# Kernel optimization log

Hardware: AMD Instinct MI355X
Metric: run time of the kernel (lower is better)

## Reference

```python
import jax, jax.numpy as jnp
import numpy as np

N = 50000      # nodes
E = 800000     # edges
IN = 128       # input feature dim
H = 4          # attention heads
D = 32         # per-head hidden dim
L = 3          # GAT layers
C = 32         # num classes
SLOPE = 0.2    # leaky relu negative slope


def _glorot(key, shape):
    fan_in, fan_out = shape[0], shape[-1]
    std = np.sqrt(2.0 / (fan_in + fan_out))
    return jax.random.normal(key, shape, dtype=jnp.float32) * std


def setup_inputs() -> dict:
    key = jax.random.key(0)
    ks = jax.random.split(key, 16)
    inp = {
        "x": jax.random.normal(ks[0], (N, IN), dtype=jnp.float32),
        "src": jax.random.randint(ks[1], (E,), 0, N, dtype=jnp.int32),
        "dst": jax.random.randint(ks[2], (E,), 0, N, dtype=jnp.int32),
        # layer 0: in_dim -> H*D
        "W0": _glorot(ks[3], (IN, H * D)),
        "al0": _glorot(ks[4], (H, D)),
        "ar0": _glorot(ks[5], (H, D)),
        # layers 1,2: H*D -> H*D
        "W1": _glorot(ks[6], (H * D, H * D)),
        "al1": _glorot(ks[7], (H, D)),
        "ar1": _glorot(ks[8], (H, D)),
        "W2": _glorot(ks[9], (H * D, H * D)),
        "al2": _glorot(ks[10], (H, D)),
        "ar2": _glorot(ks[11], (H, D)),
        # JK concat projection: L*H*D -> C (bias=False)
        "Wproj": _glorot(ks[12], (L * H * D, C)),
    }
    return inp


def gat_layer(h, W, al, ar, src, dst):
    """DGL-style GATConv (no residual, no dropout), ELU activation."""
    feat = (h @ W).reshape(N, H, D)                      # [N,H,D]
    el = jnp.sum(feat * al, axis=-1)                     # [N,H]
    er = jnp.sum(feat * ar, axis=-1)                     # [N,H]
    e = jax.nn.leaky_relu(el[src] + er[dst], negative_slope=SLOPE)  # [E,H]
    # edge softmax over incoming edges per destination node
    m = jax.lax.stop_gradient(jax.ops.segment_max(e, dst, num_segments=N))
    ex = jnp.exp(e - m[dst])                             # [E,H]
    s = jax.ops.segment_sum(ex, dst, num_segments=N)     # [N,H]
    a = ex / s[dst]                                      # [E,H]
    out = jax.ops.segment_sum(feat[src] * a[:, :, None], dst, num_segments=N)
    return jax.nn.elu(out).reshape(N, H * D)             # flatten(1)


def reference(x, src, dst, W0, al0, ar0, W1, al1, ar1, W2, al2, ar2, Wproj):
    h0 = gat_layer(x, W0, al0, ar0, src, dst)
    h1 = gat_layer(h0, W1, al1, ar1, src, dst)
    h2 = gat_layer(h1, W2, al2, ar2, src, dst)
    emb = jnp.concatenate([h0, h1, h2], axis=1)          # [N, L*H*D]
    logits = emb @ Wproj                                 # [N, C]
    return logits
```

## Files before the change

### kernel.cpp

```cpp
#include <hip/hip_runtime.h>
#include <hip/hip_fp16.h>
#include <math.h>

#define NNODES 50000
#define NEDGES 800000
#define HD     128
#define NHEADS 4
#define DH     32

#define TILE_R 64
#define AKPF   136

#define PTILE  128

#define NBUCK  196
#define BCAP   6144
#define P1_T   512
#define P1_EPB 4096
#define P2_T   512

struct alignas(16) Half8 { __half2 a, b, c, d; };
typedef _Float16 f16x8 __attribute__((ext_vector_type(8)));
typedef float    f32x4 __attribute__((ext_vector_type(4)));
typedef float    f32x8 __attribute__((ext_vector_type(8)));

static __device__ __forceinline__ float lrelu(float x){ return x > 0.f ? x : 0.2f*x; }
static __device__ __forceinline__ float elu(float x){ return x > 0.f ? x : __expf(x) - 1.f; }


__global__ void init_btail_kernel(int* btail){
  int b = blockIdx.x*blockDim.x + threadIdx.x;
  if (b < NBUCK) btail[b] = b*BCAP;
}

__global__ __launch_bounds__(P1_T) void p1_bucket_kernel(
    const int* __restrict__ src, const int* __restrict__ dst,
    int* __restrict__ btail, unsigned int* __restrict__ bstage, int e)
{
  __shared__ int cnt[NBUCK];
  __shared__ int gstart[NBUCK];
  int t = threadIdx.x;
  int base = blockIdx.x * P1_EPB;
  for (int i = t; i < NBUCK; i += P1_T) cnt[i] = 0;
  __syncthreads();
  int s_[8], b_[8], dl_[8];
  #pragma unroll
  for (int j = 0; j < 8; j++){
    int i = base + j*P1_T + t;
    if (i < e){
      int d = dst[i];
      s_[j]  = src[i];
      b_[j]  = d >> 8;
      dl_[j] = d & 255;
      atomicAdd(&cnt[b_[j]], 1);
    } else b_[j] = -1;
  }
  __syncthreads();
  for (int i = t; i < NBUCK; i += P1_T){
    gstart[i] = cnt[i] ? atomicAdd(&btail[i], cnt[i]) : 0;
    cnt[i] = 0;
  }
  __syncthreads();
  #pragma unroll
  for (int j = 0; j < 8; j++){
    if (b_[j] >= 0){
      int p = atomicAdd(&cnt[b_[j]], 1);
      bstage[(size_t)gstart[b_[j]] + p] = ((unsigned)dl_[j] << 16) | (unsigned)s_[j];
    }
  }
}

__global__ void bucket_scan_kernel(const int* __restrict__ btail, int* __restrict__ ebase,
                                   int* __restrict__ rowptr){
  if (blockIdx.x == 0 && threadIdx.x == 0){
    int run = 0;
    for (int b = 0; b < NBUCK; b++){
      ebase[b] = run;
      run += btail[b] - b*BCAP;
    }
    rowptr[NNODES] = run;
  }
}

__global__ __launch_bounds__(P2_T) void p2_csr_kernel(
    const unsigned int* __restrict__ bstage, const int* __restrict__ btail,
    const int* __restrict__ ebase, int* __restrict__ rowptr, int* __restrict__ srcs)
{
  __shared__ unsigned int ebuf[BCAP];
  __shared__ unsigned short sorted[BCAP];
  __shared__ int cnt[256], ofs[256], run[256];
  int b = blockIdx.x, t = threadIdx.x;
  int nE = btail[b] - b*BCAP;
  int gb = ebase[b];
  const unsigned int* bp = bstage + (size_t)b*BCAP;

  for (int i = t; i < 256; i += P2_T) cnt[i] = 0;
  __syncthreads();
  for (int i = t; i < nE; i += P2_T){
    unsigned int v = bp[i];
    ebuf[i] = v;
    atomicAdd(&cnt[v >> 16], 1);
  }
  __syncthreads();
  if (t < 256) ofs[t] = cnt[t];
  __syncthreads();
  for (int off = 1; off < 256; off <<= 1){
    int v = 0;
    if (t < 256 && t >= off) v = ofs[t - off];
    __syncthreads();
    if (t < 256) ofs[t] += v;
    __syncthreads();
  }
  if (t < 256){
    int ex = ofs[t] - cnt[t];
    run[t] = ex;
    int node = b*256 + t;
    if (node < NNODES) rowptr[node] = gb + ex;
  }
  __syncthreads();
  for (int i = t; i < nE; i += P2_T){
    unsigned int v = ebuf[i];
    int p = atomicAdd(&run[v >> 16], 1);
    sorted[p] = (unsigned short)(v & 0xFFFFu);
  }
  __syncthreads();
  for (int i = t; i < nE; i += P2_T)
    srcs[gb + i] = (int)sorted[i];
}

__global__ void wprep_kernel(const float* __restrict__ W0, const float* __restrict__ W1,
                             const float* __restrict__ W2, _Float16* __restrict__ wt){
  int id = blockIdx.x*blockDim.x + threadIdx.x;
  if (id >= 3*16384) return;
  int l = id >> 14, rem = id & 16383;
  int n = rem >> 7, k = rem & 127;
  const float* W = (l==0) ? W0 : (l==1) ? W1 : W2;
  wt[(size_t)l*16384 + n*128 + k] = (_Float16)W[k*128 + n];
}

template<bool FP16IN>
__global__ __launch_bounds__(256) void gemm_feat_kernel(
    const void* __restrict__ hin, int hstride,
    const _Float16* __restrict__ Wt,
    const float* __restrict__ al, const float* __restrict__ ar,
    __half* __restrict__ feat, float* __restrict__ elv, float* __restrict__ erv)
{
  __shared__ __align__(16) _Float16 Ah[TILE_R*AKPF];
  __shared__ __align__(16) _Float16 Wh[HD*AKPF];
  int t = threadIdx.x;
  int w = t >> 6, lane = t & 63;
  int c = lane & 15, quad = lane >> 4;
  int rbase = blockIdx.x * TILE_R;

  f32x4 acc[8];
  #pragma unroll
  for (int ct = 0; ct < 8; ct++) acc[ct] = (f32x4){0.f, 0.f, 0.f, 0.f};

  int arow = t >> 2;
  int akq  = t & 3;
  int an   = rbase + arow;
  if (FP16IN){
    const _Float16* ap = (const _Float16*)hin + (size_t)an*hstride + akq*8;
    #pragma unroll
    for (int kb = 0; kb < HD; kb += 32){
      f16x8 av = (f16x8)((_Float16)0);
      if (an < NNODES) av = *(const f16x8*)(ap + kb);
      *(f16x8*)&Ah[arow*AKPF + kb + akq*8] = av;
    }
  } else {
    const float* ap = (const float*)hin + (size_t)an*hstride + akq*8;
    #pragma unroll
    for (int kb = 0; kb < HD; kb += 32){
      float4 v0 = make_float4(0.f,0.f,0.f,0.f), v1 = v0;
      if (an < NNODES){
        v0 = *(const float4*)(ap + kb);
        v1 = *(const float4*)(ap + kb + 4);
      }
      f16x8 av;
      av[0]=(_Float16)v0.x; av[1]=(_Float16)v0.y; av[2]=(_Float16)v0.z; av[3]=(_Float16)v0.w;
      av[4]=(_Float16)v1.x; av[5]=(_Float16)v1.y; av[6]=(_Float16)v1.z; av[7]=(_Float16)v1.w;
      *(f16x8*)&Ah[arow*AKPF + kb + akq*8] = av;
    }
  }
  int wn = t >> 1;
  int wk = (t & 1) * 16;
  const _Float16* wp = Wt + wn*HD + wk;
  #pragma unroll
  for (int kb = 0; kb < HD; kb += 32){
    *(uint4*)&Wh[wn*AKPF + kb + wk]     = *(const uint4*)(wp + kb);
    *(uint4*)&Wh[wn*AKPF + kb + wk + 8] = *(const uint4*)(wp + kb + 8);
  }
  __syncthreads();

  #pragma unroll
  for (int kb = 0; kb < HD; kb += 32){
    f16x8 afrag = *(const f16x8*)&Ah[(w*16 + c)*AKPF + kb + quad*8];
    #pragma unroll
    for (int ct = 0; ct < 8; ct++){
      f16x8 bfrag = *(const f16x8*)&Wh[(ct*16 + c)*AKPF + kb + quad*8];
      acc[ct] = __builtin_amdgcn_mfma_f32_16x16x32_f16(afrag, bfrag, acc[ct], 0, 0, 0);
    }
  }

  float alv[8], arv[8];
  #pragma unroll
  for (int ct = 0; ct < 8; ct++){
    int idx = (ct >> 1)*DH + (ct & 1)*16 + c;
    alv[ct] = al[idx];
    arv[ct] = ar[idx];
  }
  #pragma unroll
  for (int r = 0; r < 4; r++){
    int n = rbase + w*16 + quad*4 + r;
    float pl[4], pr[4];
    #pragma unroll
    for (int hh = 0; hh < 4; hh++){
      pl[hh] = acc[2*hh][r]*alv[2*hh] + acc[2*hh+1][r]*alv[2*hh+1];
      pr[hh] = acc[2*hh][r]*arv[2*hh] + acc[2*hh+1][r]*arv[2*hh+1];
    }
    #pragma unroll
    for (int hh = 0; hh < 4; hh++){
      pl[hh] += __shfl_xor(pl[hh], 1); pl[hh] += __shfl_xor(pl[hh], 2);
      pl[hh] += __shfl_xor(pl[hh], 4); pl[hh] += __shfl_xor(pl[hh], 8);
      pr[hh] += __shfl_xor(pr[hh], 1); pr[hh] += __shfl_xor(pr[hh], 2);
      pr[hh] += __shfl_xor(pr[hh], 4); pr[hh] += __shfl_xor(pr[hh], 8);
    }
    if (n < NNODES){
      if (c < 4){ elv[n*NHEADS + c] = pl[c]; erv[n*NHEADS + c] = pr[c]; }
      #pragma unroll
      for (int ct = 0; ct < 8; ct++)
        feat[(size_t)n*HD + ct*16 + c] = __float2half_rn(acc[ct][r]);
    }
  }
}

#define MIX2(alo, ahi, pk, aa) \
  asm("v_fma_mix_f32 %0, %2, %3, %0 op_sel:[0,0,0] op_sel_hi:[1,0,0]\n\t" \
      "v_fma_mix_f32 %1, %2, %3, %1 op_sel:[1,0,0] op_sel_hi:[1,0,0]" \
      : "+v"(alo), "+v"(ahi) : "v"(pk), "v"(aa))

__global__ __launch_bounds__(256) void smax_agg_kernel(
    const int* __restrict__ rowptr, const int* __restrict__ srcs,
    const float* __restrict__ elv, const float* __restrict__ erv,
    const __half* __restrict__ feat, __half* __restrict__ emb_out, int n)
{
  int gid = (int)((blockIdx.x*(size_t)blockDim.x + threadIdx.x) >> 3);
  if (gid >= n) return;
  int fl8  = threadIdx.x & 7;
  int fo   = fl8 * 16;
  int head = fl8 >> 1;

  int s0 = rowptr[gid], s1 = rowptr[gid+1];
  float erh = erv[gid*4 + head];

  float acc[16];
  #pragma unroll
  for (int j = 0; j < 16; j++) acc[j] = 0.f;
  float ssum = 0.f;

  const uint4 zq = make_uint4(0,0,0,0);

  int   sA[4], sB[4];
  uint4 qA0[4], qA1[4], qB0[4], qB1[4];
  float eA[4], eB[4];

#define LOADB(base, S, Q0, Q1, EL)                                   \
  {                                                                  \
    _Pragma("unroll")                                                \
    for (int j = 0; j < 4; j++){                                     \
      int ee = (base) + j;                                           \
      S[j] = (ee < s1) ? srcs[ee] : -1;                              \
    }                                                                \
    _Pragma("unroll")                                                \
    for (int j = 0; j < 4; j++){                                     \
      if (S[j] >= 0){                                                \
        const __half* fr = feat + ((size_t)S[j] << 7) + fo;          \
        Q0[j] = *(const uint4*)(fr);                                 \
        Q1[j] = *(const uint4*)(fr + 8);                             \
        EL[j] = elv[S[j]*4 + head];                                  \
      } else { Q0[j] = zq; Q1[j] = zq; EL[j] = 0.f; }                \
    }                                                                \
  }

#define ACCB(S, Q0, Q1, EL)                                          \
  {                                                                  \
    _Pragma("unroll")                                                \
    for (int j = 0; j < 4; j++){                                     \
      float x = EL[j] + erh;                                         \
      float a = (S[j] >= 0) ? __expf(fmaxf(x, 0.2f*x)) : 0.f;        \
      ssum += a;                                                     \
      MIX2(acc[0],  acc[1],  Q0[j].x, a);                            \
      MIX2(acc[2],  acc[3],  Q0[j].y, a);                            \
      MIX2(acc[4],  acc[5],  Q0[j].z, a);                            \
      MIX2(acc[6],  acc[7],  Q0[j].w, a);                            \
      MIX2(acc[8],  acc[9],  Q1[j].x, a);                            \
      MIX2(acc[10], acc[11], Q1[j].y, a);                            \
      MIX2(acc[12], acc[13], Q1[j].z, a);                            \
      MIX2(acc[14], acc[15], Q1[j].w, a);                            \
    }                                                                \
  }

  LOADB(s0, sA, qA0, qA1, eA);
  for (int e = s0; e < s1; e += 8){
    LOADB(e + 4, sB, qB0, qB1, eB);
    ACCB(sA, qA0, qA1, eA);
    LOADB(e + 8, sA, qA0, qA1, eA);
    ACCB(sB, qB0, qB1, eB);
  }
#undef LOADB
#undef ACCB

  float inv = (ssum > 0.f) ? 1.f / ssum : 0.f;
  __half2 hv[8];
  #pragma unroll
  for (int j = 0; j < 8; j++)
    hv[j] = __floats2half2_rn(elu(acc[2*j]*inv), elu(acc[2*j+1]*inv));
  __half* op = emb_out + (size_t)gid*384 + fo;
  *(uint4*)(op)     = *(uint4*)&hv[0];
  *(uint4*)(op + 8) = *(uint4*)&hv[4];
}

__global__ __launch_bounds__(256) void proj_kernel(
    const __half* __restrict__ emb, const float* __restrict__ Wp, float* __restrict__ part)
{
  __shared__ float As[PTILE*36];
  __shared__ float Wl[32*32];
  int t = threadIdx.x;
  int tx = t & 3, ty = t >> 2;
  int rbase = blockIdx.x * PTILE;
  int kstart = blockIdx.y * 192;
  float* pout = part + (size_t)blockIdx.y * NNODES * 32;

  float acc[2][8];
  #pragma unroll
  for (int r = 0; r < 2; r++)
    #pragma unroll
    for (int j = 0; j < 8; j++) acc[r][j] = 0.f;

  for (int kb = kstart; kb < kstart + 192; kb += 32){
    #pragma unroll
    for (int i = 0; i < 2; i++){
      int idx = i*256 + t;
      int row = idx >> 2;
      int kq  = (idx & 3) * 8;
      int gr  = rbase + row;
      f16x8 v = (f16x8)((_Float16)0);
      if (gr < NNODES) v = *(const f16x8*)((const _Float16*)emb + (size_t)gr*384 + kb + kq);
      float4 f0, f1;
      f0.x=(float)v[0]; f0.y=(float)v[1]; f0.z=(float)v[2]; f0.w=(float)v[3];
      f1.x=(float)v[4]; f1.y=(float)v[5]; f1.z=(float)v[6]; f1.w=(float)v[7];
      *(float4*)&As[row*36 + kq]     = f0;
      *(float4*)&As[row*36 + kq + 4] = f1;
    }
    *(float4*)&Wl[t*4] = *(const float4*)(Wp + (size_t)kb*32 + t*4);
    __syncthreads();

    #pragma unroll 8
    for (int k = 0; k < 32; k++){
      float4 b0 = *(const float4*)&Wl[k*32 + tx*8];
      float4 b1 = *(const float4*)&Wl[k*32 + tx*8 + 4];
      #pragma unroll
      for (int r = 0; r < 2; r++){
        float a = As[(ty + 64*r)*36 + k];
        acc[r][0] += a*b0.x; acc[r][1] += a*b0.y;
        acc[r][2] += a*b0.z; acc[r][3] += a*b0.w;
        acc[r][4] += a*b1.x; acc[r][5] += a*b1.y;
        acc[r][6] += a*b1.z; acc[r][7] += a*b1.w;
      }
    }
    __syncthreads();
  }

  #pragma unroll
  for (int r = 0; r < 2; r++){
    int n = rbase + ty + 64*r;
    if (n < NNODES){
      *(float4*)(pout + (size_t)n*32 + tx*8)     = make_float4(acc[r][0], acc[r][1], acc[r][2], acc[r][3]);
      *(float4*)(pout + (size_t)n*32 + tx*8 + 4) = make_float4(acc[r][4], acc[r][5], acc[r][6], acc[r][7]);
    }
  }
}

__global__ void proj_reduce_kernel(const float4* __restrict__ part, float4* __restrict__ out, int n4){
  int i = blockIdx.x*blockDim.x + threadIdx.x;
  if (i >= n4) return;
  float4 a = part[i];
  float4 b = part[n4 + i];
  out[i] = make_float4(a.x + b.x, a.y + b.y, a.z + b.z, a.w + b.w);
}

extern "C" void kernel_launch(void* const* d_in, const int* in_sizes, int n_in,
                              void* d_out, int out_size, void* d_ws, size_t ws_size,
                              hipStream_t stream) {
  const float* x    = (const float*)d_in[0];
  const int*   src  = (const int*)d_in[1];
  const int*   dst  = (const int*)d_in[2];
  const float* Ws_[3]  = { (const float*)d_in[3], (const float*)d_in[6], (const float*)d_in[9]  };
  const float* als[3] = { (const float*)d_in[4], (const float*)d_in[7], (const float*)d_in[10] };
  const float* ars[3] = { (const float*)d_in[5], (const float*)d_in[8], (const float*)d_in[11] };
  const float* Wproj  = (const float*)d_in[12];
  float* out = (float*)d_out;

  char* wptr = (char*)d_ws;
  auto alloc = [&](size_t bytes) -> void* {
    void* p = (void*)wptr; wptr += (bytes + 255) & ~(size_t)255; return p;
  };
  int*      btail      = (int*)     alloc((size_t)NBUCK*4);
  int*      ebase      = (int*)     alloc((size_t)NBUCK*4);
  unsigned* bstage     = (unsigned*)alloc((size_t)NBUCK*BCAP*4);
  int*      rowptr     = (int*)     alloc((size_t)(NNODES+1)*4);
  int*      src_sorted = (int*)     alloc((size_t)NEDGES*4);
  __half*   feat       = (__half*)  alloc((size_t)NNODES*HD*2);
  float*    elv        = (float*)   alloc((size_t)NNODES*NHEADS*4);
  float*    erv        = (float*)   alloc((size_t)NNODES*NHEADS*4);
  __half*   emb        = (__half*)  alloc((size_t)NNODES*384*2);
  float*    part       = (float*)   alloc((size_t)2*NNODES*32*4);
  _Float16* wt         = (_Float16*)alloc((size_t)3*HD*HD*2);

  init_btail_kernel<<<1, 256, 0, stream>>>(btail);
  p1_bucket_kernel<<<(NEDGES + P1_EPB - 1)/P1_EPB, P1_T, 0, stream>>>(
      src, dst, btail, bstage, NEDGES);
  bucket_scan_kernel<<<1, 64, 0, stream>>>(btail, ebase, rowptr);
  p2_csr_kernel<<<NBUCK, P2_T, 0, stream>>>(bstage, btail, ebase, rowptr, src_sorted);

  wprep_kernel<<<(3*HD*HD + 255)/256, 256, 0, stream>>>(Ws_[0], Ws_[1], Ws_[2], wt);

  const int NGB = (NNODES + TILE_R - 1)/TILE_R;
  const int NSMB = (NNODES*8 + 255)/256;
  gemm_feat_kernel<false><<<NGB, 256, 0, stream>>>(
      (const void*)x, 128, wt, als[0], ars[0], feat, elv, erv);
  smax_agg_kernel<<<NSMB, 256, 0, stream>>>(rowptr, src_sorted, elv, erv,
                                            feat, emb, NNODES);
  for (int l = 1; l < 3; l++){
    gemm_feat_kernel<true><<<NGB, 256, 0, stream>>>(
        (const void*)(emb + (size_t)(l-1)*128), 384,
        wt + (size_t)l*HD*HD, als[l], ars[l], feat, elv, erv);
    smax_agg_kernel<<<NSMB, 256, 0, stream>>>(rowptr, src_sorted, elv, erv,
                                              feat, emb + (size_t)l*128, NNODES);
  }

  dim3 pgrid((NNODES + PTILE - 1)/PTILE, 2);
  proj_kernel<<<pgrid, 256, 0, stream>>>(emb, Wproj, part);
  const int OUT4 = NNODES*32/4;
  proj_reduce_kernel<<<(OUT4+255)/256, 256, 0, stream>>>((const float4*)part, (float4*)out, OUT4);
}
```

Measured before the change: 299.5 us.

## Sort nodes by in-degree for load-balanced softmax aggregation

Builds a degree histogram while constructing the CSR, then computes a prefix over degree bins and scatters node ids into a degree-sorted permutation. The aggregation kernel processes nodes in that order, so neighbouring 8-lane groups in a wavefront have similar edge counts and less divergence. The serial bucket scan is also replaced with a parallel shared-memory scan. The cost is two extra small kernels plus an indirection that breaks contiguity of rowptr, erv and output writes.

```diff
diff --git a/kernel.cpp b/kernel.cpp
--- a/kernel.cpp
+++ b/kernel.cpp
@@ -19,6 +19,8 @@
 #define P1_EPB 4096
 #define P2_T   512
 
+#define NDBIN  64
+
 struct alignas(16) Half8 { __half2 a, b, c, d; };
 typedef _Float16 f16x8 __attribute__((ext_vector_type(8)));
 typedef float    f32x4 __attribute__((ext_vector_type(4)));
@@ -28,9 +30,10 @@
 static __device__ __forceinline__ float elu(float x){ return x > 0.f ? x : __expf(x) - 1.f; }
 
 
-__global__ void init_btail_kernel(int* btail){
+__global__ void init_btail_kernel(int* btail, int* gdhist){
   int b = blockIdx.x*blockDim.x + threadIdx.x;
   if (b < NBUCK) btail[b] = b*BCAP;
+  if (b < NDBIN) gdhist[b] = 0;
 }
 
 __global__ __launch_bounds__(P1_T) void p1_bucket_kernel(
@@ -70,31 +73,41 @@
   }
 }
 
-__global__ void bucket_scan_kernel(const int* __restrict__ btail, int* __restrict__ ebase,
-                                   int* __restrict__ rowptr){
-  if (blockIdx.x == 0 && threadIdx.x == 0){
-    int run = 0;
-    for (int b = 0; b < NBUCK; b++){
-      ebase[b] = run;
-      run += btail[b] - b*BCAP;
-    }
-    rowptr[NNODES] = run;
-  }
+__global__ __launch_bounds__(256) void bucket_scan_kernel(
+    const int* __restrict__ btail, int* __restrict__ ebase, int* __restrict__ rowptr)
+{
+  __shared__ int c[256];
+  int t = threadIdx.x;
+  int mine = (t < NBUCK) ? (btail[t] - t*BCAP) : 0;
+  c[t] = mine;
+  __syncthreads();
+  for (int off = 1; off < 256; off <<= 1){
+    int v = 0;
+    if (t >= off) v = c[t - off];
+    __syncthreads();
+    c[t] += v;
+    __syncthreads();
+  }
+  if (t < NBUCK) ebase[t] = c[t] - mine;
+  if (t == NBUCK - 1) rowptr[NNODES] = c[t];
 }
 
 __global__ __launch_bounds__(P2_T) void p2_csr_kernel(
     const unsigned int* __restrict__ bstage, const int* __restrict__ btail,
-    const int* __restrict__ ebase, int* __restrict__ rowptr, int* __restrict__ srcs)
+    const int* __restrict__ ebase, int* __restrict__ rowptr, int* __restrict__ srcs,
+    int* __restrict__ gdhist)
 {
   __shared__ unsigned int ebuf[BCAP];
   __shared__ unsigned short sorted[BCAP];
   __shared__ int cnt[256], ofs[256], run[256];
+  __shared__ int dh[NDBIN];
   int b = blockIdx.x, t = threadIdx.x;
   int nE = btail[b] - b*BCAP;
   int gb = ebase[b];
   const unsigned int* bp = bstage + (size_t)b*BCAP;
 
   for (int i = t; i < 256; i += P2_T) cnt[i] = 0;
+  if (t < NDBIN) dh[t] = 0;
   __syncthreads();
   for (int i = t; i < nE; i += P2_T){
     unsigned int v = bp[i];
@@ -115,9 +128,14 @@
     int ex = ofs[t] - cnt[t];
     run[t] = ex;
     int node = b*256 + t;
-    if (node < NNODES) rowptr[node] = gb + ex;
-  }
-  __syncthreads();
+    if (node < NNODES){
+      rowptr[node] = gb + ex;
+      int dbin = cnt[t] > NDBIN-1 ? NDBIN-1 : cnt[t];
+      atomicAdd(&dh[dbin], 1);
+    }
+  }
+  __syncthreads();
+  if (t < NDBIN && dh[t]) atomicAdd(&gdhist[t], dh[t]);
   for (int i = t; i < nE; i += P2_T){
     unsigned int v = ebuf[i];
     int p = atomicAdd(&run[v >> 16], 1);
@@ -126,6 +144,44 @@
   __syncthreads();
   for (int i = t; i < nE; i += P2_T)
     srcs[gb + i] = (int)sorted[i];
+}
+
+__global__ void dprefix_kernel(const int* __restrict__ gdhist, int* __restrict__ run){
+  __shared__ int c[NDBIN];
+  int t = threadIdx.x;
+  int mine = gdhist[t];
+  c[t] = mine;
+  __syncthreads();
+  for (int off = 1; off < NDBIN; off <<= 1){
+    int v = 0;
+    if (t >= off) v = c[t - off];
+    __syncthreads();
+    c[t] += v;
+    __syncthreads();
+  }
+  run[t] = c[t] - mine;
+}
+
+__global__ __launch_bounds__(256) void perm_scatter_kernel(
+    const int* __restrict__ rowptr, int* __restrict__ run, int* __restrict__ perm)
+{
+  __shared__ int lh[NDBIN], bb[NDBIN];
+  int t = threadIdx.x, node = blockIdx.x*256 + t;
+  if (t < NDBIN) lh[t] = 0;
+  __syncthreads();
+  int dbin = -1;
+  if (node < NNODES){
+    int d = rowptr[node+1] - rowptr[node];
+    dbin = d > NDBIN-1 ? NDBIN-1 : d;
+    atomicAdd(&lh[dbin], 1);
+  }
+  __syncthreads();
+  if (t < NDBIN){ bb[t] = lh[t] ? atomicAdd(&run[t], lh[t]) : 0; lh[t] = 0; }
+  __syncthreads();
+  if (dbin >= 0){
+    int r = atomicAdd(&lh[dbin], 1);
+    perm[bb[dbin] + r] = node;
+  }
 }
 
 __global__ void wprep_kernel(const float* __restrict__ W0, const float* __restrict__ W1,
@@ -241,11 +297,13 @@
 
 __global__ __launch_bounds__(256) void smax_agg_kernel(
     const int* __restrict__ rowptr, const int* __restrict__ srcs,
+    const int* __restrict__ perm,
     const float* __restrict__ elv, const float* __restrict__ erv,
     const __half* __restrict__ feat, __half* __restrict__ emb_out, int n)
 {
-  int gid = (int)((blockIdx.x*(size_t)blockDim.x + threadIdx.x) >> 3);
-  if (gid >= n) return;
+  int g = (int)((blockIdx.x*(size_t)blockDim.x + threadIdx.x) >> 3);
+  if (g >= n) return;
+  int gid = perm[g];
   int fl8  = threadIdx.x & 7;
   int fo   = fl8 * 16;
   int head = fl8 >> 1;
@@ -416,12 +474,17 @@
   __half*   emb        = (__half*)  alloc((size_t)NNODES*384*2);
   float*    part       = (float*)   alloc((size_t)2*NNODES*32*4);
   _Float16* wt         = (_Float16*)alloc((size_t)3*HD*HD*2);
-
-  init_btail_kernel<<<1, 256, 0, stream>>>(btail);
+  int*      gdhist     = (int*)     alloc((size_t)NDBIN*4);
+  int*      drun       = (int*)     alloc((size_t)NDBIN*4);
+  int*      perm       = (int*)     alloc((size_t)NNODES*4);
+
+  init_btail_kernel<<<1, 256, 0, stream>>>(btail, gdhist);
   p1_bucket_kernel<<<(NEDGES + P1_EPB - 1)/P1_EPB, P1_T, 0, stream>>>(
       src, dst, btail, bstage, NEDGES);
-  bucket_scan_kernel<<<1, 64, 0, stream>>>(btail, ebase, rowptr);
-  p2_csr_kernel<<<NBUCK, P2_T, 0, stream>>>(bstage, btail, ebase, rowptr, src_sorted);
+  bucket_scan_kernel<<<1, 256, 0, stream>>>(btail, ebase, rowptr);
+  p2_csr_kernel<<<NBUCK, P2_T, 0, stream>>>(bstage, btail, ebase, rowptr, src_sorted, gdhist);
+  dprefix_kernel<<<1, NDBIN, 0, stream>>>(gdhist, drun);
+  perm_scatter_kernel<<<NBUCK, 256, 0, stream>>>(rowptr, drun, perm);
 
   wprep_kernel<<<(3*HD*HD + 255)/256, 256, 0, stream>>>(Ws_[0], Ws_[1], Ws_[2], wt);
 
@@ -429,13 +492,13 @@
   const int NSMB = (NNODES*8 + 255)/256;
   gemm_feat_kernel<false><<<NGB, 256, 0, stream>>>(
       (const void*)x, 128, wt, als[0], ars[0], feat, elv, erv);
-  smax_agg_kernel<<<NSMB, 256, 0, stream>>>(rowptr, src_sorted, elv, erv,
+  smax_agg_kernel<<<NSMB, 256, 0, stream>>>(rowptr, src_sorted, perm, elv, erv,
                                             feat, emb, NNODES);
   for (int l = 1; l < 3; l++){
     gemm_feat_kernel<true><<<NGB, 256, 0, stream>>>(
         (const void*)(emb + (size_t)(l-1)*128), 384,
         wt + (size_t)l*HD*HD, als[l], ars[l], feat, elv, erv);
-    smax_agg_kernel<<<NSMB, 256, 0, stream>>>(rowptr, src_sorted, elv, erv,
+    smax_agg_kernel<<<NSMB, 256, 0, stream>>>(rowptr, src_sorted, perm, elv, erv,
                                               feat, emb + (size_t)l*128, NNODES);
   }
 
```

After: 304.8 us. Within noise of the previous version (+1.8%).

## Use MFMA for final projection, fuse weight prep and parallelize bucket scan

Applied to the files above, without the earlier changes.

Replaces the scalar FP32 split-K projection plus its reduce kernel with a single MFMA fp16 kernel that keeps the whole transposed projection weight in shared memory and writes output directly. Merges btail init, layer weight transposition and projection weight conversion into one prep kernel. Replaces the single-thread bucket scan with a 256-thread shared-memory scan. These cut launches, the partial-sum buffer traffic and scalar FMA cost, at the price of fp16 weight rounding for the projection.

```diff
diff --git a/kernel.cpp b/kernel.cpp
--- a/kernel.cpp
+++ b/kernel.cpp
@@ -11,8 +11,6 @@
 #define TILE_R 64
 #define AKPF   136
 
-#define PTILE  128
-
 #define NBUCK  196
 #define BCAP   6144
 #define P1_T   512
@@ -27,11 +25,24 @@
 static __device__ __forceinline__ float lrelu(float x){ return x > 0.f ? x : 0.2f*x; }
 static __device__ __forceinline__ float elu(float x){ return x > 0.f ? x : __expf(x) - 1.f; }
 
-
-__global__ void init_btail_kernel(int* btail){
-  int b = blockIdx.x*blockDim.x + threadIdx.x;
-  if (b < NBUCK) btail[b] = b*BCAP;
-}
+__global__ void prep_kernel(const float* __restrict__ W0, const float* __restrict__ W1,
+                            const float* __restrict__ W2, const float* __restrict__ Wp,
+                            _Float16* __restrict__ wt, _Float16* __restrict__ wt2,
+                            int* __restrict__ btail){
+  int id = blockIdx.x*blockDim.x + threadIdx.x;
+  if (id < NBUCK) btail[id] = id*BCAP;
+  if (id < 3*16384){
+    int l = id >> 14, rem = id & 16383;
+    int n = rem >> 7, k = rem & 127;
+    const float* W = (l==0) ? W0 : (l==1) ? W1 : W2;
+    wt[(size_t)l*16384 + n*128 + k] = (_Float16)W[k*128 + n];
+  } else if (id < 3*16384 + 12288){
+    int rem = id - 3*16384;
+    int k = rem >> 5, n = rem & 31;
+    wt2[n*384 + k] = (_Float16)Wp[k*32 + n];
+  }
+}
+
 
 __global__ __launch_bounds__(P1_T) void p1_bucket_kernel(
     const int* __restrict__ src, const int* __restrict__ dst,
@@ -70,16 +81,23 @@
   }
 }
 
-__global__ void bucket_scan_kernel(const int* __restrict__ btail, int* __restrict__ ebase,
-                                   int* __restrict__ rowptr){
-  if (blockIdx.x == 0 && threadIdx.x == 0){
-    int run = 0;
-    for (int b = 0; b < NBUCK; b++){
-      ebase[b] = run;
-      run += btail[b] - b*BCAP;
-    }
-    rowptr[NNODES] = run;
-  }
+__global__ __launch_bounds__(256) void bucket_scan_kernel(
+    const int* __restrict__ btail, int* __restrict__ ebase, int* __restrict__ rowptr)
+{
+  __shared__ int c[256];
+  int t = threadIdx.x;
+  int mine = (t < NBUCK) ? (btail[t] - t*BCAP) : 0;
+  c[t] = mine;
+  __syncthreads();
+  for (int off = 1; off < 256; off <<= 1){
+    int v = 0;
+    if (t >= off) v = c[t - off];
+    __syncthreads();
+    c[t] += v;
+    __syncthreads();
+  }
+  if (t < NBUCK) ebase[t] = c[t] - mine;
+  if (t == NBUCK - 1) rowptr[NNODES] = c[t];
 }
 
 __global__ __launch_bounds__(P2_T) void p2_csr_kernel(
@@ -126,16 +144,6 @@
   __syncthreads();
   for (int i = t; i < nE; i += P2_T)
     srcs[gb + i] = (int)sorted[i];
-}
-
-__global__ void wprep_kernel(const float* __restrict__ W0, const float* __restrict__ W1,
-                             const float* __restrict__ W2, _Float16* __restrict__ wt){
-  int id = blockIdx.x*blockDim.x + threadIdx.x;
-  if (id >= 3*16384) return;
-  int l = id >> 14, rem = id & 16383;
-  int n = rem >> 7, k = rem & 127;
-  const float* W = (l==0) ? W0 : (l==1) ? W1 : W2;
-  wt[(size_t)l*16384 + n*128 + k] = (_Float16)W[k*128 + n];
 }
 
 template<bool FP16IN>
@@ -320,73 +328,68 @@
   *(uint4*)(op + 8) = *(uint4*)&hv[4];
 }
 
-__global__ __launch_bounds__(256) void proj_kernel(
-    const __half* __restrict__ emb, const float* __restrict__ Wp, float* __restrict__ part)
-{
-  __shared__ float As[PTILE*36];
-  __shared__ float Wl[32*32];
+__global__ __launch_bounds__(256) void proj_mfma_kernel(
+    const __half* __restrict__ emb, const _Float16* __restrict__ Wt2,
+    float* __restrict__ out)
+{
+  __shared__ __align__(16) _Float16 Ah[128*136];
+  __shared__ __align__(16) _Float16 Bh[32*392];
   int t = threadIdx.x;
-  int tx = t & 3, ty = t >> 2;
-  int rbase = blockIdx.x * PTILE;
-  int kstart = blockIdx.y * 192;
-  float* pout = part + (size_t)blockIdx.y * NNODES * 32;
-
-  float acc[2][8];
-  #pragma unroll
-  for (int r = 0; r < 2; r++)
-    #pragma unroll
-    for (int j = 0; j < 8; j++) acc[r][j] = 0.f;
-
-  for (int kb = kstart; kb < kstart + 192; kb += 32){
-    #pragma unroll
-    for (int i = 0; i < 2; i++){
+  int w = t >> 6, lane = t & 63;
+  int c = lane & 15, quad = lane >> 4;
+  int rbase = blockIdx.x * 128;
+
+  f32x4 acc[2][2];
+  #pragma unroll
+  for (int rt = 0; rt < 2; rt++)
+    #pragma unroll
+    for (int ct = 0; ct < 2; ct++) acc[rt][ct] = (f32x4){0.f,0.f,0.f,0.f};
+
+  #pragma unroll
+  for (int i = 0; i < 6; i++){
+    int idx = i*256 + t;
+    int row = idx / 48;
+    int q8  = idx - row*48;
+    *(f16x8*)&Bh[row*392 + q8*8] = *(const f16x8*)(Wt2 + row*384 + q8*8);
+  }
+
+  for (int kc = 0; kc < 384; kc += 128){
+    #pragma unroll
+    for (int i = 0; i < 8; i++){
       int idx = i*256 + t;
-      int row = idx >> 2;
-      int kq  = (idx & 3) * 8;
+      int row = idx >> 4;
+      int q   = idx & 15;
       int gr  = rbase + row;
       f16x8 v = (f16x8)((_Float16)0);
-      if (gr < NNODES) v = *(const f16x8*)((const _Float16*)emb + (size_t)gr*384 + kb + kq);
-      float4 f0, f1;
-      f0.x=(float)v[0]; f0.y=(float)v[1]; f0.z=(float)v[2]; f0.w=(float)v[3];
-      f1.x=(float)v[4]; f1.y=(float)v[5]; f1.z=(float)v[6]; f1.w=(float)v[7];
-      *(float4*)&As[row*36 + kq]     = f0;
-      *(float4*)&As[row*36 + kq + 4] = f1;
-    }
-    *(float4*)&Wl[t*4] = *(const float4*)(Wp + (size_t)kb*32 + t*4);
-    __syncthreads();
-
-    #pragma unroll 8
-    for (int k = 0; k < 32; k++){
-      float4 b0 = *(const float4*)&Wl[k*32 + tx*8];
-      float4 b1 = *(const float4*)&Wl[k*32 + tx*8 + 4];
+      if (gr < NNODES) v = *(const f16x8*)((const _Float16*)emb + (size_t)gr*384 + kc + q*8);
+      *(f16x8*)&Ah[row*136 + q*8] = v;
+    }
+    __syncthreads();
+    #pragma unroll
+    for (int kb = 0; kb < 128; kb += 32){
       #pragma unroll
-      for (int r = 0; r < 2; r++){
-        float a = As[(ty + 64*r)*36 + k];
-        acc[r][0] += a*b0.x; acc[r][1] += a*b0.y;
-        acc[r][2] += a*b0.z; acc[r][3] += a*b0.w;
-        acc[r][4] += a*b1.x; acc[r][5] += a*b1.y;
-        acc[r][6] += a*b1.z; acc[r][7] += a*b1.w;
+      for (int rt = 0; rt < 2; rt++){
+        f16x8 afrag = *(const f16x8*)&Ah[(w*32 + rt*16 + c)*136 + kb + quad*8];
+        #pragma unroll
+        for (int ct = 0; ct < 2; ct++){
+          f16x8 bfrag = *(const f16x8*)&Bh[(ct*16 + c)*392 + kc + kb + quad*8];
+          acc[rt][ct] = __builtin_amdgcn_mfma_f32_16x16x32_f16(afrag, bfrag, acc[rt][ct], 0, 0, 0);
+        }
       }
     }
     __syncthreads();
   }
 
   #pragma unroll
-  for (int r = 0; r < 2; r++){
-    int n = rbase + ty + 64*r;
-    if (n < NNODES){
-      *(float4*)(pout + (size_t)n*32 + tx*8)     = make_float4(acc[r][0], acc[r][1], acc[r][2], acc[r][3]);
-      *(float4*)(pout + (size_t)n*32 + tx*8 + 4) = make_float4(acc[r][4], acc[r][5], acc[r][6], acc[r][7]);
-    }
-  }
-}
-
-__global__ void proj_reduce_kernel(const float4* __restrict__ part, float4* __restrict__ out, int n4){
-  int i = blockIdx.x*blockDim.x + threadIdx.x;
-  if (i >= n4) return;
-  float4 a = part[i];
-  float4 b = part[n4 + i];
-  out[i] = make_float4(a.x + b.x, a.y + b.y, a.z + b.z, a.w + b.w);
+  for (int rt = 0; rt < 2; rt++)
+    #pragma unroll
+    for (int r = 0; r < 4; r++){
+      int n = rbase + w*32 + rt*16 + quad*4 + r;
+      if (n < NNODES){
+        out[(size_t)n*32 + c]      = acc[rt][0][r];
+        out[(size_t)n*32 + 16 + c] = acc[rt][1][r];
+      }
+    }
 }
 
 extern "C" void kernel_launch(void* const* d_in, const int* in_sizes, int n_in,
@@ -414,16 +417,16 @@
   float*    elv        = (float*)   alloc((size_t)NNODES*NHEADS*4);
   float*    erv        = (float*)   alloc((size_t)NNODES*NHEADS*4);
   __half*   emb        = (__half*)  alloc((size_t)NNODES*384*2);
-  float*    part       = (float*)   alloc((size_t)2*NNODES*32*4);
   _Float16* wt         = (_Float16*)alloc((size_t)3*HD*HD*2);
-
-  init_btail_kernel<<<1, 256, 0, stream>>>(btail);
+  _Float16* wt2        = (_Float16*)alloc((size_t)32*384*2);
+
+  prep_kernel<<<(3*16384 + 12288 + 255)/256, 256, 0, stream>>>(
+      Ws_[0], Ws_[1], Ws_[2], Wproj, wt, wt2, btail);
+
   p1_bucket_kernel<<<(NEDGES + P1_EPB - 1)/P1_EPB, P1_T, 0, stream>>>(
       src, dst, btail, bstage, NEDGES);
-  bucket_scan_kernel<<<1, 64, 0, stream>>>(btail, ebase, rowptr);
+  bucket_scan_kernel<<<1, 256, 0, stream>>>(btail, ebase, rowptr);
   p2_csr_kernel<<<NBUCK, P2_T, 0, stream>>>(bstage, btail, ebase, rowptr, src_sorted);
-
-  wprep_kernel<<<(3*HD*HD + 255)/256, 256, 0, stream>>>(Ws_[0], Ws_[1], Ws_[2], wt);
 
   const int NGB = (NNODES + TILE_R - 1)/TILE_R;
   const int NSMB = (NNODES*8 + 255)/256;
@@ -439,8 +442,5 @@
                                               feat, emb + (size_t)l*128, NNODES);
   }
 
-  dim3 pgrid((NNODES + PTILE - 1)/PTILE, 2);
-  proj_kernel<<<pgrid, 256, 0, stream>>>(emb, Wproj, part);
-  const int OUT4 = NNODES*32/4;
-  proj_reduce_kernel<<<(OUT4+255)/256, 256, 0, stream>>>((const float4*)part, (float4*)out, OUT4);
-}
+  proj_mfma_kernel<<<(NNODES + 127)/128, 256, 0, stream>>>(emb, wt2, out);
+}
```

New measurement: 273.1 us. 8.8% less time.
